# Performance work log

Hardware: AMD Instinct MI355X
Metric: run time of the kernel (lower is better)

The kernel has to match this reference:

```python
import jax, jax.numpy as jnp
import numpy as np

N = 40000          # nodes
E = 640000         # edges
F = 128            # feature_size
H = 4              # heads
D = 128 // 4       # out_channels per head (transformer_dim // heads)
V = 64             # label_vocab


def setup_inputs() -> dict:
    key = jax.random.key(0)
    ks = jax.random.split(key, 16)
    s = 1.0 / np.sqrt(F)
    return {
        "x": jax.random.normal(ks[0], (N, F), dtype=jnp.float32),
        "y": jax.random.randint(ks[1], (N, 1), 0, V, dtype=jnp.int64),
        "edge_index": jax.random.randint(ks[2], (2, E), 0, N, dtype=jnp.int64),
        "emb": jax.random.normal(ks[3], (V, F), dtype=jnp.float32),
        "Wq": jax.random.uniform(ks[4], (F, H * D), jnp.float32, -s, s),
        "bq": jnp.zeros((H * D,), jnp.float32),
        "Wk": jax.random.uniform(ks[5], (F, H * D), jnp.float32, -s, s),
        "bk": jnp.zeros((H * D,), jnp.float32),
        "Wv": jax.random.uniform(ks[6], (F, H * D), jnp.float32, -s, s),
        "bv": jnp.zeros((H * D,), jnp.float32),
        "Ws": jax.random.uniform(ks[7], (F, H * D), jnp.float32, -s, s),
        "bs": jnp.zeros((H * D,), jnp.float32),
        "Wl": jax.random.uniform(ks[8], (H * D, V), jnp.float32, -1.0 / np.sqrt(H * D), 1.0 / np.sqrt(H * D)),
        "bl": jnp.zeros((V,), jnp.float32),
    }


def reference(x, y, edge_index, emb, Wq, bq, Wk, bk, Wv, bv, Ws, bs, Wl, bl):
    # label embedding + add
    x_y = x + emb[y.squeeze(-1)]                      # [N, F]

    # per-node Q/K/V projections
    q = (x_y @ Wq + bq).reshape(N, H, D)
    k = (x_y @ Wk + bk).reshape(N, H, D)
    v = (x_y @ Wv + bv).reshape(N, H, D)

    src = edge_index[0]                               # source nodes j
    dst = edge_index[1]                               # target nodes i

    # edge-wise attention logits: (q_i . k_j) / sqrt(D)  -> [E, H]
    alpha = jnp.einsum('ehd,ehd->eh', q[dst], k[src]) / jnp.sqrt(jnp.asarray(D, x.dtype))

    # segment softmax over incoming edges of each target node
    m = jax.ops.segment_max(alpha, dst, num_segments=N)          # [N, H]
    ea = jnp.exp(alpha - m[dst])                                 # [E, H]
    denom = jax.ops.segment_sum(ea, dst, num_segments=N)         # [N, H]
    w = ea / denom[dst]                                          # [E, H]

    # weighted message aggregation (scatter-add over dst)
    msg = w[:, :, None] * v[src]                                 # [E, H, D]
    out = jax.ops.segment_sum(msg, dst, num_segments=N)          # [N, H, D]
    out = out.reshape(N, H * D)

    # root/skip connection (PyG root_weight=True default)
    out = out + (x_y @ Ws + bs)

    # final classifier
    return out @ Wl + bl                                         # [N, V]
```

## Files before the change

### kernel.cpp

```cpp
#include <hip/hip_runtime.h>
#include <hip/hip_bf16.h>

#define NN 40000
#define NN64 40064
#define EE 640000
#define CAP 64
#define NBKT 157
#define BKTCAP 4608
#define NFB 314
#define EPB1 2039

typedef __attribute__((ext_vector_type(8))) short short8;
typedef __attribute__((ext_vector_type(4))) float floatx4;

__device__ inline unsigned short f2bf(float f) {
    unsigned u = __float_as_uint(f);
    unsigned r = (u + 0x7FFFu + ((u >> 16) & 1u)) >> 16;
    return (unsigned short)r;
}
__device__ inline float bflo(unsigned u) { return __uint_as_float(u << 16); }
__device__ inline float bfhi(unsigned u) { return __uint_as_float(u & 0xFFFF0000u); }

__global__ void pack_kernel(const float* __restrict__ Wq, const float* __restrict__ Wk,
                            const float* __restrict__ Wv, const float* __restrict__ Ws,
                            unsigned short* __restrict__ Wp, int* __restrict__ gcur) {
    int idx = blockIdx.x * 256 + threadIdx.x;
    if (idx < 65536) {
        int mode = idx >> 14;
        int r = idx & 16383;
        int n = r >> 7, k = r & 127;
        const float* W = (mode == 0) ? Wq : (mode == 1) ? Wk : (mode == 2) ? Wv : Ws;
        float val = W[k * 128 + n];
        if (mode == 0) val *= 0.17677669529663687f;
        Wp[idx] = f2bf(val);
    }
    if (idx < NBKT) gcur[idx] = 0;
}

__global__ __launch_bounds__(256) void fill_kernel(
    const int* __restrict__ ei, int* __restrict__ gcur,
    unsigned* __restrict__ bucketed) {
    __shared__ int lcnt[NBKT], lbase[NBKT];
    int bid = blockIdx.x;
    int t = threadIdx.x;
    if (t < NBKT) lcnt[t] = 0;
    __syncthreads();
    int e0 = bid * EPB1;
    unsigned key[8];
#pragma unroll
    for (int k = 0; k < 8; ++k) {
        int o = k * 256 + t;
        int e = e0 + o;
        unsigned kk = 0xFFFFFFFFu;
        if (o < EPB1 && e < EE) {
            int d = ei[EE + e];
            int s = ei[e];
            kk = ((unsigned)d << 16) | (unsigned)s;
            atomicAdd(&lcnt[d >> 8], 1);
        }
        key[k] = kk;
    }
    __syncthreads();
    if (t < NBKT) lbase[t] = atomicAdd(&gcur[t], lcnt[t]);
    __syncthreads();
    if (t < NBKT) lcnt[t] = 0;
    __syncthreads();
#pragma unroll
    for (int k = 0; k < 8; ++k) {
        unsigned kk = key[k];
        if (kk != 0xFFFFFFFFu) {
            int b = kk >> 24;
            int off = atomicAdd(&lcnt[b], 1);
            int pos = lbase[b] + off;
            if (pos < BKTCAP) bucketed[b * BKTCAP + pos] = kk;
        }
    }
}

__global__ __launch_bounds__(256) void csr_build(
    const unsigned* __restrict__ bucketed, const int* __restrict__ gcur,
    unsigned short* __restrict__ csr, int* __restrict__ cnt) {
    __shared__ int dcnt[256];
    int b = blockIdx.x, t = threadIdx.x;
    dcnt[t] = 0;
    __syncthreads();
    int nb = gcur[b];
    if (nb > BKTCAP) nb = BKTCAP;
    const unsigned* src = bucketed + b * BKTCAP;
    for (int i = t; i < nb; i += 256) {
        unsigned kk = src[i];
        int d = kk >> 16;
        int pos = atomicAdd(&dcnt[d & 255], 1);
        if (pos < CAP) csr[((size_t)d << 6) + pos] = (unsigned short)(kk & 0xFFFFu);
    }
    __syncthreads();
    int d = b * 256 + t;
    if (d < NN) cnt[d] = min(dcnt[t], CAP);
}

__global__ __launch_bounds__(256) void gemm_kernel(
    const float4* __restrict__ x4, const int* __restrict__ yy,
    const float4* __restrict__ emb4, const unsigned short* __restrict__ Wp,
    const float* __restrict__ bq, const float* __restrict__ bk,
    const float* __restrict__ bv, const float* __restrict__ bs,
    unsigned* __restrict__ qss, unsigned* __restrict__ kvd) {
    __shared__ unsigned short As[16 * 136];
    long m0 = (long)blockIdx.x * 16;

    {
        int t = threadIdx.x;
        int row = t >> 4, seg = t & 15;
        long gr = m0 + row;
        uint4 o;
        if (gr < NN) {
            int yv = yy[gr];
            float4 a0 = x4[gr * 32 + seg * 2];
            float4 a1 = x4[gr * 32 + seg * 2 + 1];
            float4 b0 = emb4[(long)yv * 32 + seg * 2];
            float4 b1 = emb4[(long)yv * 32 + seg * 2 + 1];
            o.x = f2bf(a0.x + b0.x) | ((unsigned)f2bf(a0.y + b0.y) << 16);
            o.y = f2bf(a0.z + b0.z) | ((unsigned)f2bf(a0.w + b0.w) << 16);
            o.z = f2bf(a1.x + b1.x) | ((unsigned)f2bf(a1.y + b1.y) << 16);
            o.w = f2bf(a1.z + b1.z) | ((unsigned)f2bf(a1.w + b1.w) << 16);
        } else {
            o.x = 0; o.y = 0; o.z = 0; o.w = 0;
        }
        *(uint4*)&As[row * 136 + seg * 8] = o;
    }
    __syncthreads();

    int w  = threadIdx.x >> 6;
    int ln = threadIdx.x & 15;
    int qd = (threadIdx.x & 63) >> 4;

    short8 afr[4];
#pragma unroll
    for (int kc = 0; kc < 4; ++kc)
        afr[kc] = *(const short8*)&As[ln * 136 + kc * 32 + qd * 8];

    long row = m0 + ln;
    bool rowok = (row < NN);
    int ni0 = w * 2;

    unsigned lo[2][4];
#pragma unroll
    for (int pass = 0; pass < 4; ++pass) {
        const int mode = (pass == 0) ? 0 : (pass == 1) ? 3 : (pass == 2) ? 1 : 2;
        const unsigned short* Wm = Wp + (size_t)mode * 16384;
        const float* bb = (pass == 0) ? bq : (pass == 1) ? bs : (pass == 2) ? bk : bv;
        float bsc = (pass == 0) ? 0.17677669529663687f : 1.0f;

        floatx4 acc[2];
#pragma unroll
        for (int j = 0; j < 2; ++j) acc[j] = (floatx4){0.f, 0.f, 0.f, 0.f};
#pragma unroll
        for (int kc = 0; kc < 4; ++kc) {
            short8 bfr[2];
#pragma unroll
            for (int j = 0; j < 2; ++j)
                bfr[j] = *(const short8*)&Wm[((ni0 + j) * 16 + ln) * 128 + kc * 32 + qd * 8];
#pragma unroll
            for (int j = 0; j < 2; ++j)
                acc[j] = __builtin_amdgcn_mfma_f32_16x16x32_bf16(
                    bfr[j], afr[kc], acc[j], 0, 0, 0);
        }
        if (pass == 0 || pass == 2) {
#pragma unroll
            for (int j = 0; j < 2; ++j) {
                int col0 = (ni0 + j) * 16 + qd * 4;
                float4 bv4 = *(const float4*)&bb[col0];
                lo[j][0] = f2bf(acc[j][0] + bv4.x * bsc);
                lo[j][1] = f2bf(acc[j][1] + bv4.y * bsc);
                lo[j][2] = f2bf(acc[j][2] + bv4.z * bsc);
                lo[j][3] = f2bf(acc[j][3] + bv4.w * bsc);
            }
        } else {
            unsigned* dst = (pass == 1) ? qss : kvd;
            if (rowok) {
#pragma unroll
                for (int j = 0; j < 2; ++j) {
                    int col0 = (ni0 + j) * 16 + qd * 4;
                    float4 bv4 = *(const float4*)&bb[col0];
                    uint4 o;
                    o.x = lo[j][0] | ((unsigned)f2bf(acc[j][0] + bv4.x) << 16);
                    o.y = lo[j][1] | ((unsigned)f2bf(acc[j][1] + bv4.y) << 16);
                    o.z = lo[j][2] | ((unsigned)f2bf(acc[j][2] + bv4.z) << 16);
                    o.w = lo[j][3] | ((unsigned)f2bf(acc[j][3] + bv4.w) << 16);
                    *(uint4*)&dst[row * 128 + col0] = o;
                }
            }
        }
    }
}

__global__ __launch_bounds__(256) void attn_kernel(
    const unsigned* __restrict__ qss, const uint4* __restrict__ kv4,
    const int* __restrict__ cnt_g, const unsigned short* __restrict__ csr,
    const float* __restrict__ Wl, const float* __restrict__ bl,
    float* __restrict__ out) {
    __shared__ float P[8][128];
    __shared__ float red[4][8][64];
    int w = threadIdx.x >> 6;
    int lane = threadIdx.x & 63;
    int half = lane >> 5;
    int node = w * 2 + half;
    int i = blockIdx.x * 8 + node;
    int l5 = lane & 31;
    uint4 qu = ((const uint4*)qss)[i * 32 + l5];
    float q0 = bflo(qu.x), q1 = bflo(qu.y), q2 = bflo(qu.z), q3 = bflo(qu.w);
    float s0 = bfhi(qu.x), s1 = bfhi(qu.y), s2 = bfhi(qu.z), s3 = bfhi(qu.w);
    int cnt = cnt_g[i];
    if (cnt > CAP) cnt = CAP;
    const unsigned short* lst = csr + (i << 6);
    int cntA = __shfl(cnt, 0, 64);
    int cntB = __shfl(cnt, 32, 64);
    int cntmax = (cntA > cntB) ? cntA : cntB;

    float m = -3.0e38f, l = 0.f, a0 = 0.f, a1 = 0.f, a2 = 0.f, a3 = 0.f;
    for (int p = 0; p < cntmax; p += 8) {
        uint4 jj = *(const uint4*)&lst[p];
        int j0 = min((int)(jj.x & 0xFFFFu), NN - 1);
        int j1 = min((int)(jj.x >> 16),     NN - 1);
        int j2 = min((int)(jj.y & 0xFFFFu), NN - 1);
        int j3 = min((int)(jj.y >> 16),     NN - 1);
        int j4 = min((int)(jj.z & 0xFFFFu), NN - 1);
        int j5 = min((int)(jj.z >> 16),     NN - 1);
        int j6 = min((int)(jj.w & 0xFFFFu), NN - 1);
        int j7 = min((int)(jj.w >> 16),     NN - 1);
        uint4 u0 = kv4[j0 * 32 + l5];
        uint4 u1 = kv4[j1 * 32 + l5];
        uint4 u2 = kv4[j2 * 32 + l5];
        uint4 u3 = kv4[j3 * 32 + l5];
        uint4 u4 = kv4[j4 * 32 + l5];
        uint4 u5 = kv4[j5 * 32 + l5];
        uint4 u6 = kv4[j6 * 32 + l5];
        uint4 u7 = kv4[j7 * 32 + l5];
        float pr0 = fmaf(q3, bflo(u0.w), fmaf(q2, bflo(u0.z), fmaf(q1, bflo(u0.y), q0 * bflo(u0.x))));
        float pr1 = fmaf(q3, bflo(u1.w), fmaf(q2, bflo(u1.z), fmaf(q1, bflo(u1.y), q0 * bflo(u1.x))));
        float pr2 = fmaf(q3, bflo(u2.w), fmaf(q2, bflo(u2.z), fmaf(q1, bflo(u2.y), q0 * bflo(u2.x))));
        float pr3 = fmaf(q3, bflo(u3.w), fmaf(q2, bflo(u3.z), fmaf(q1, bflo(u3.y), q0 * bflo(u3.x))));
        float pr4 = fmaf(q3, bflo(u4.w), fmaf(q2, bflo(u4.z), fmaf(q1, bflo(u4.y), q0 * bflo(u4.x))));
        float pr5 = fmaf(q3, bflo(u5.w), fmaf(q2, bflo(u5.z), fmaf(q1, bflo(u5.y), q0 * bflo(u5.x))));
        float pr6 = fmaf(q3, bflo(u6.w), fmaf(q2, bflo(u6.z), fmaf(q1, bflo(u6.y), q0 * bflo(u6.x))));
        float pr7 = fmaf(q3, bflo(u7.w), fmaf(q2, bflo(u7.z), fmaf(q1, bflo(u7.y), q0 * bflo(u7.x))));
#pragma unroll
        for (int s = 4; s; s >>= 1) {
            pr0 += __shfl_xor(pr0, s, 64);
            pr1 += __shfl_xor(pr1, s, 64);
            pr2 += __shfl_xor(pr2, s, 64);
            pr3 += __shfl_xor(pr3, s, 64);
            pr4 += __shfl_xor(pr4, s, 64);
            pr5 += __shfl_xor(pr5, s, 64);
            pr6 += __shfl_xor(pr6, s, 64);
            pr7 += __shfl_xor(pr7, s, 64);
        }
        pr0 = (p + 0 < cnt) ? pr0 : -3.0e38f;
        pr1 = (p + 1 < cnt) ? pr1 : -3.0e38f;
        pr2 = (p + 2 < cnt) ? pr2 : -3.0e38f;
        pr3 = (p + 3 < cnt) ? pr3 : -3.0e38f;
        pr4 = (p + 4 < cnt) ? pr4 : -3.0e38f;
        pr5 = (p + 5 < cnt) ? pr5 : -3.0e38f;
        pr6 = (p + 6 < cnt) ? pr6 : -3.0e38f;
        pr7 = (p + 7 < cnt) ? pr7 : -3.0e38f;
        float mnew = fmaxf(m, fmaxf(fmaxf(fmaxf(pr0, pr1), fmaxf(pr2, pr3)),
                                    fmaxf(fmaxf(pr4, pr5), fmaxf(pr6, pr7))));
        float sc = __expf(m - mnew);
        float e0 = __expf(pr0 - mnew), e1 = __expf(pr1 - mnew);
        float e2 = __expf(pr2 - mnew), e3 = __expf(pr3 - mnew);
        float e4 = __expf(pr4 - mnew), e5 = __expf(pr5 - mnew);
        float e6 = __expf(pr6 - mnew), e7 = __expf(pr7 - mnew);
        l  = l * sc + ((e0 + e1) + (e2 + e3)) + ((e4 + e5) + (e6 + e7));
        a0 = fmaf(e3, bfhi(u3.x), fmaf(e2, bfhi(u2.x), fmaf(e1, bfhi(u1.x), fmaf(e0, bfhi(u0.x), a0 * sc))));
        a0 = fmaf(e7, bfhi(u7.x), fmaf(e6, bfhi(u6.x), fmaf(e5, bfhi(u5.x), fmaf(e4, bfhi(u4.x), a0))));
        a1 = fmaf(e3, bfhi(u3.y), fmaf(e2, bfhi(u2.y), fmaf(e1, bfhi(u1.y), fmaf(e0, bfhi(u0.y), a1 * sc))));
        a1 = fmaf(e7, bfhi(u7.y), fmaf(e6, bfhi(u6.y), fmaf(e5, bfhi(u5.y), fmaf(e4, bfhi(u4.y), a1))));
        a2 = fmaf(e3, bfhi(u3.z), fmaf(e2, bfhi(u2.z), fmaf(e1, bfhi(u1.z), fmaf(e0, bfhi(u0.z), a2 * sc))));
        a2 = fmaf(e7, bfhi(u7.z), fmaf(e6, bfhi(u6.z), fmaf(e5, bfhi(u5.z), fmaf(e4, bfhi(u4.z), a2))));
        a3 = fmaf(e3, bfhi(u3.w), fmaf(e2, bfhi(u2.w), fmaf(e1, bfhi(u1.w), fmaf(e0, bfhi(u0.w), a3 * sc))));
        a3 = fmaf(e7, bfhi(u7.w), fmaf(e6, bfhi(u6.w), fmaf(e5, bfhi(u5.w), fmaf(e4, bfhi(u4.w), a3))));
        m = mnew;
    }
    float inv = (cnt > 0 && l > 0.f) ? (1.0f / l) : 0.f;
    float4 po;
    po.x = a0 * inv + s0;
    po.y = a1 * inv + s1;
    po.z = a2 * inv + s2;
    po.w = a3 * inv + s3;
    *(float4*)&P[node][l5 * 4] = po;
    __syncthreads();

    {
        int col = lane;
        const float* WlW = Wl + (size_t)(w * 32) * 64 + col;
        float c[8];
#pragma unroll
        for (int n = 0; n < 8; ++n) c[n] = 0.f;
#pragma unroll 8
        for (int kk = 0; kk < 32; ++kk) {
            float wl = WlW[kk * 64];
            int k = w * 32 + kk;
#pragma unroll
            for (int n = 0; n < 8; ++n) c[n] = fmaf(P[n][k], wl, c[n]);
        }
#pragma unroll
        for (int n = 0; n < 8; ++n) red[w][n][col] = c[n];
    }
    __syncthreads();

#pragma unroll
    for (int t = threadIdx.x; t < 512; t += 256) {
        int n = t >> 6, col = t & 63;
        float s = red[0][n][col] + red[1][n][col] + red[2][n][col] + red[3][n][col];
        out[(long)(blockIdx.x * 8 + n) * 64 + col] = s + bl[col];
    }
}

extern "C" void kernel_launch(void* const* d_in, const int* in_sizes, int n_in,
                              void* d_out, int out_size, void* d_ws, size_t ws_size,
                              hipStream_t stream) {
    const float* x   = (const float*)d_in[0];
    const int*   y   = (const int*)d_in[1];
    const int*   ei  = (const int*)d_in[2];
    const float* emb = (const float*)d_in[3];
    const float* Wq  = (const float*)d_in[4];  const float* bq = (const float*)d_in[5];
    const float* Wk  = (const float*)d_in[6];  const float* bk = (const float*)d_in[7];
    const float* Wv  = (const float*)d_in[8];  const float* bv = (const float*)d_in[9];
    const float* Wsk = (const float*)d_in[10]; const float* bs = (const float*)d_in[11];
    const float* Wl  = (const float*)d_in[12]; const float* bl = (const float*)d_in[13];
    float* out = (float*)d_out;

    char* w = (char*)d_ws;
    unsigned*       qss  = (unsigned*)(w);
    unsigned*       kv   = (unsigned*)(w + 20480000);
    unsigned short* csr  = (unsigned short*)(w + 40960000);
    unsigned short* Wp   = (unsigned short*)(w + 46080000);
    unsigned*   bucketed = (unsigned*)(w + 46211072);
    int*            gcur = (int*)(w + 49104896);
    int*            cnt  = (int*)(w + 49105920);

    pack_kernel<<<256, 256, 0, stream>>>(Wq, Wk, Wv, Wsk, Wp, gcur);
    fill_kernel<<<NFB, 256, 0, stream>>>(ei, gcur, bucketed);
    csr_build<<<NBKT, 256, 0, stream>>>(bucketed, gcur, csr, cnt);
    gemm_kernel<<<NN64 / 16, 256, 0, stream>>>((const float4*)x, y, (const float4*)emb,
                                               Wp, bq, bk, bv, bs, qss, kv);
    attn_kernel<<<NN / 8, 256, 0, stream>>>(qss, (const uint4*)kv, cnt, csr,
                                            Wl, bl, out);
}
```

Baseline: 208.6 us.

## Merge CSR build into GEMM launch and shrink attention blocks to four nodes

The CSR bucket-to-row build and the QKV/skip GEMM now run as one launch, with block index dispatching to either role. This saves one kernel launch and lets the two independent stages overlap on the GPU. The attention kernel moves to 128-thread blocks handling four nodes, and each wave computes the full 128-deep output projection for its own two nodes. That drops the cross-wave reduction buffer and one barrier, at the cost of a longer per-thread loop and more Wl reloads per block.

```diff
diff --git a/kernel.cpp b/kernel.cpp
--- a/kernel.cpp
+++ b/kernel.cpp
@@ -9,6 +9,7 @@
 #define BKTCAP 4608
 #define NFB 314
 #define EPB1 2039
+#define NGB 2504
 
 typedef __attribute__((ext_vector_type(8))) short short8;
 typedef __attribute__((ext_vector_type(4))) float floatx4;
@@ -77,35 +78,37 @@
     }
 }
 
-__global__ __launch_bounds__(256) void csr_build(
+__global__ __launch_bounds__(256) void csrbuild_gemm(
     const unsigned* __restrict__ bucketed, const int* __restrict__ gcur,
-    unsigned short* __restrict__ csr, int* __restrict__ cnt) {
-    __shared__ int dcnt[256];
-    int b = blockIdx.x, t = threadIdx.x;
-    dcnt[t] = 0;
-    __syncthreads();
-    int nb = gcur[b];
-    if (nb > BKTCAP) nb = BKTCAP;
-    const unsigned* src = bucketed + b * BKTCAP;
-    for (int i = t; i < nb; i += 256) {
-        unsigned kk = src[i];
-        int d = kk >> 16;
-        int pos = atomicAdd(&dcnt[d & 255], 1);
-        if (pos < CAP) csr[((size_t)d << 6) + pos] = (unsigned short)(kk & 0xFFFFu);
-    }
-    __syncthreads();
-    int d = b * 256 + t;
-    if (d < NN) cnt[d] = min(dcnt[t], CAP);
-}
-
-__global__ __launch_bounds__(256) void gemm_kernel(
+    unsigned short* __restrict__ csr, int* __restrict__ cnt,
     const float4* __restrict__ x4, const int* __restrict__ yy,
     const float4* __restrict__ emb4, const unsigned short* __restrict__ Wp,
     const float* __restrict__ bq, const float* __restrict__ bk,
     const float* __restrict__ bv, const float* __restrict__ bs,
     unsigned* __restrict__ qss, unsigned* __restrict__ kvd) {
+    __shared__ int dcnt[256];
     __shared__ unsigned short As[16 * 136];
-    long m0 = (long)blockIdx.x * 16;
+
+    if (blockIdx.x < NBKT) {
+        int b = blockIdx.x, t = threadIdx.x;
+        dcnt[t] = 0;
+        __syncthreads();
+        int nb = gcur[b];
+        if (nb > BKTCAP) nb = BKTCAP;
+        const unsigned* src = bucketed + b * BKTCAP;
+        for (int i = t; i < nb; i += 256) {
+            unsigned kk = src[i];
+            int d = kk >> 16;
+            int pos = atomicAdd(&dcnt[d & 255], 1);
+            if (pos < CAP) csr[((size_t)d << 6) + pos] = (unsigned short)(kk & 0xFFFFu);
+        }
+        __syncthreads();
+        int d = b * 256 + t;
+        if (d < NN) cnt[d] = min(dcnt[t], CAP);
+        return;
+    }
+
+    long m0 = (long)(blockIdx.x - NBKT) * 16;
 
     {
         int t = threadIdx.x;
@@ -193,18 +196,17 @@
     }
 }
 
-__global__ __launch_bounds__(256) void attn_kernel(
+__global__ __launch_bounds__(128) void attn_kernel(
     const unsigned* __restrict__ qss, const uint4* __restrict__ kv4,
     const int* __restrict__ cnt_g, const unsigned short* __restrict__ csr,
     const float* __restrict__ Wl, const float* __restrict__ bl,
     float* __restrict__ out) {
-    __shared__ float P[8][128];
-    __shared__ float red[4][8][64];
-    int w = threadIdx.x >> 6;
+    __shared__ float P[4][128];
+    int wid = threadIdx.x >> 6;
     int lane = threadIdx.x & 63;
     int half = lane >> 5;
-    int node = w * 2 + half;
-    int i = blockIdx.x * 8 + node;
+    int node = wid * 2 + half;
+    int i = blockIdx.x * 4 + node;
     int l5 = lane & 31;
     uint4 qu = ((const uint4*)qss)[i * 32 + l5];
     float q0 = bflo(qu.x), q1 = bflo(qu.y), q2 = bflo(qu.z), q3 = bflo(qu.w);
@@ -291,27 +293,19 @@
 
     {
         int col = lane;
-        const float* WlW = Wl + (size_t)(w * 32) * 64 + col;
-        float c[8];
-#pragma unroll
-        for (int n = 0; n < 8; ++n) c[n] = 0.f;
+        int n0 = wid * 2, n1 = wid * 2 + 1;
+        const float* WlC = Wl + col;
+        float c0 = 0.f, c1 = 0.f;
 #pragma unroll 8
-        for (int kk = 0; kk < 32; ++kk) {
-            float wl = WlW[kk * 64];
-            int k = w * 32 + kk;
-#pragma unroll
-            for (int n = 0; n < 8; ++n) c[n] = fmaf(P[n][k], wl, c[n]);
-        }
-#pragma unroll
-        for (int n = 0; n < 8; ++n) red[w][n][col] = c[n];
-    }
-    __syncthreads();
-
-#pragma unroll
-    for (int t = threadIdx.x; t < 512; t += 256) {
-        int n = t >> 6, col = t & 63;
-        float s = red[0][n][col] + red[1][n][col] + red[2][n][col] + red[3][n][col];
-        out[(long)(blockIdx.x * 8 + n) * 64 + col] = s + bl[col];
+        for (int k = 0; k < 128; ++k) {
+            float wl = WlC[k * 64];
+            c0 = fmaf(P[n0][k], wl, c0);
+            c1 = fmaf(P[n1][k], wl, c1);
+        }
+        float bb = bl[col];
+        long base = (long)blockIdx.x * 4;
+        out[(base + n0) * 64 + col] = c0 + bb;
+        out[(base + n1) * 64 + col] = c1 + bb;
     }
 }
 
@@ -340,9 +334,9 @@
 
     pack_kernel<<<256, 256, 0, stream>>>(Wq, Wk, Wv, Wsk, Wp, gcur);
     fill_kernel<<<NFB, 256, 0, stream>>>(ei, gcur, bucketed);
-    csr_build<<<NBKT, 256, 0, stream>>>(bucketed, gcur, csr, cnt);
-    gemm_kernel<<<NN64 / 16, 256, 0, stream>>>((const float4*)x, y, (const float4*)emb,
-                                               Wp, bq, bk, bv, bs, qss, kv);
-    attn_kernel<<<NN / 8, 256, 0, stream>>>(qss, (const uint4*)kv, cnt, csr,
+    csrbuild_gemm<<<NBKT + NGB, 256, 0, stream>>>(
+        bucketed, gcur, csr, cnt,
+        (const float4*)x, y, (const float4*)emb, Wp, bq, bk, bv, bs, qss, kv);
+    attn_kernel<<<NN / 4, 128, 0, stream>>>(qss, (const uint4*)kv, cnt, csr,
                                             Wl, bl, out);
 }
```

Result: no change. 208.1 us (-0.2%).
